# Kernel optimization log

Measured on AMD Instinct MI355X. Metric: run time of the kernel, lower is better.

The kernel has to match this reference:

```python
import jax, jax.numpy as jnp
import numpy as np

N_NODES = 100000
N_EDGES = 1600000
IN_CH = 128
HID = 32
N_GRAPHS = 64


def _gcn_conv(x, src, dst, W, b, n_nodes):
    # PyG GCNConv defaults: x' = D^{-1/2} (A + I) D^{-1/2} (x W) + b
    h = x @ W                                   # [N, out]
    loop = jnp.arange(n_nodes, dtype=src.dtype)
    s = jnp.concatenate([src, loop])            # add self-loops
    d = jnp.concatenate([dst, loop])
    deg = jax.ops.segment_sum(jnp.ones_like(d, dtype=h.dtype), d, num_segments=n_nodes)
    dinv = jnp.where(deg > 0, jax.lax.rsqrt(deg), 0.0)
    norm = dinv[s] * dinv[d]                    # [E+N]
    msg = h[s] * norm[:, None]                  # gather + scale
    out = jax.ops.segment_sum(msg, d, num_segments=n_nodes)  # scatter-add
    return out + b


def setup_inputs() -> dict:
    key = jax.random.key(0)
    ks = jax.random.split(key, 8)
    x = jax.random.normal(ks[0], (N_NODES, IN_CH), dtype=jnp.float32)
    edge_index = jax.random.randint(ks[1], (2, N_EDGES), 0, N_NODES, dtype=jnp.int32)
    batch = jnp.sort(jax.random.randint(ks[2], (N_NODES,), 0, N_GRAPHS, dtype=jnp.int32))
    W1 = jax.random.normal(ks[3], (IN_CH, HID), dtype=jnp.float32) * (1.0 / np.sqrt(IN_CH))
    b1 = jnp.zeros((HID,), dtype=jnp.float32)
    W2 = jax.random.normal(ks[4], (HID, HID), dtype=jnp.float32) * (1.0 / np.sqrt(HID))
    b2 = jnp.zeros((HID,), dtype=jnp.float32)
    Ws = jax.random.normal(ks[5], (HID, HID), dtype=jnp.float32) * (1.0 / np.sqrt(HID))
    bs = jnp.zeros((HID,), dtype=jnp.float32)
    return {"x": x, "edge_index": edge_index, "batch": batch,
            "W1": W1, "b1": b1, "W2": W2, "b2": b2, "Ws": Ws, "bs": bs}


def reference(x, edge_index, batch, W1, b1, W2, b2, Ws, bs):
    src, dst = edge_index[0], edge_index[1]
    n = x.shape[0]
    h = _gcn_conv(x, src, dst, W1, b1, n)
    h = jax.nn.relu(h)
    h = _gcn_conv(h, src, dst, W2, b2, n)       # [N, HID] node embeddings
    # global_mean_pool over graph ids
    ones = jnp.ones((n,), dtype=h.dtype)
    cnt = jax.ops.segment_sum(ones, batch, num_segments=N_GRAPHS)
    gsum = jax.ops.segment_sum(h, batch, num_segments=N_GRAPHS)
    g = gsum / jnp.maximum(cnt, 1.0)[:, None]   # [G, HID]
    summary = g @ Ws + bs
    return summary, h
```

## Files before the change

### kernel.cpp

```cpp
#include <hip/hip_runtime.h>

#define N_NODES  100000
#define N_EDGES  1600000
#define IN_CH    128
#define HID      32
#define N_GRAPHS 64

#define NBIN   391
#define CHUNK  4096
#define MGRID  391
#define STG    5120
#define LCAP   2048

#define OFF_B      0
#define OFF_EDGEPK 3200000
#define OFF_CSR    4800000
#define OFF_COLT   6400000
#define OFF_BINB   6400391
#define OFF_ROWPTR 6400784
#define OFF_DINV   6500785

__device__ __forceinline__ unsigned bfr(float f) {
    unsigned u = __float_as_uint(f);
    u += 0x7fffu + ((u >> 16) & 1u);
    return u >> 16;
}
__device__ __forceinline__ float bflo(unsigned w) { return __uint_as_float(w << 16); }
__device__ __forceinline__ float bfhi(unsigned w) { return __uint_as_float(w & 0xffff0000u); }

__global__ __launch_bounds__(512) void hist_kernel(const int* __restrict__ dst,
                                                   int* __restrict__ H) {
    __shared__ int s[512];
    int t = threadIdx.x, wg = blockIdx.x;
    s[t] = 0;
    __syncthreads();
    int e0 = wg * CHUNK, e1 = min(e0 + CHUNK, N_EDGES);
    for (int e = e0 + t; e < e1; e += 512) {
        int d = dst[e];
        if ((unsigned)d < N_NODES) atomicAdd(&s[d >> 8], 1);
    }
    __syncthreads();
    if (t < NBIN) H[t * MGRID + wg] = s[t];
}

__global__ __launch_bounds__(512) void scanrow_kernel(int* __restrict__ H,
                                                      int* __restrict__ colT) {
    __shared__ int s[512];
    int t = threadIdx.x, bin = blockIdx.x;
    s[t] = (t < MGRID) ? H[bin * MGRID + t] : 0;
    __syncthreads();
    for (int off = 1; off < 512; off <<= 1) {
        int v = (t >= off) ? s[t - off] : 0;
        __syncthreads();
        if (t >= off) s[t] += v;
        __syncthreads();
    }
    if (t < MGRID) H[bin * MGRID + t] = t ? s[t - 1] : 0;
    if (t == 0) colT[bin] = s[MGRID - 1];
}

__global__ __launch_bounds__(512) void scanbase_kernel(const int* __restrict__ colT,
                                                       int* __restrict__ binB,
                                                       int* __restrict__ row_ptr) {
    __shared__ int s[512];
    int t = threadIdx.x;
    s[t] = (t < NBIN) ? colT[t] : 0;
    __syncthreads();
    for (int off = 1; off < 512; off <<= 1) {
        int v = (t >= off) ? s[t - off] : 0;
        __syncthreads();
        if (t >= off) s[t] += v;
        __syncthreads();
    }
    if (t < NBIN) binB[t] = t ? s[t - 1] : 0;
    if (t == 0) { binB[NBIN] = s[NBIN - 1]; row_ptr[N_NODES] = s[NBIN - 1]; }
}

__global__ __launch_bounds__(512) void msplit_kernel(const int* __restrict__ src,
                                                     const int* __restrict__ dst,
                                                     const int* __restrict__ H,
                                                     const int* __restrict__ binB,
                                                     int* __restrict__ edgepk) {
    __shared__ int s[512];
    __shared__ int cur[NBIN];
    __shared__ int gb[NBIN];
    __shared__ int stage[CHUNK];
    __shared__ int gof[CHUNK];
    int t = threadIdx.x, wg = blockIdx.x;
    s[t] = 0;
    __syncthreads();
    int e0 = wg * CHUNK, e1 = min(e0 + CHUNK, N_EDGES);
    for (int e = e0 + t; e < e1; e += 512) {
        int d = dst[e];
        if ((unsigned)d < N_NODES) atomicAdd(&s[d >> 8], 1);
    }
    __syncthreads();
    for (int off = 1; off < 512; off <<= 1) {
        int v = (t >= off) ? s[t - off] : 0;
        __syncthreads();
        if (t >= off) s[t] += v;
        __syncthreads();
    }
    if (t < NBIN) {
        int lo = t ? s[t - 1] : 0;
        cur[t] = lo;
        gb[t] = binB[t] + H[t * MGRID + wg] - lo;
    }
    __syncthreads();
    for (int e = e0 + t; e < e1; e += 512) {
        int d = dst[e];
        if ((unsigned)d < N_NODES) {
            int b = d >> 8;
            int p = atomicAdd(&cur[b], 1);
            stage[p] = (src[e] << 8) | (d & 255);
            gof[p] = gb[b];
        }
    }
    __syncthreads();
    int total = s[511];
    for (int p = t; p < total; p += 512)
        edgepk[gof[p] + p] = stage[p];
}

__global__ __launch_bounds__(512) void csr2_kernel(const int* __restrict__ edgepk,
                                                   const int* __restrict__ binB,
                                                   int* __restrict__ row_ptr,
                                                   float* __restrict__ dinv,
                                                   int* __restrict__ csr) {
    __shared__ int cnt[256], s[256], cur[256];
    __shared__ int stage[STG];
    int t = threadIdx.x, bin = blockIdx.x;
    int ebase = binB[bin], eend = binB[bin + 1];
    int n = eend - ebase;
    if (t < 256) cnt[t] = 0;
    __syncthreads();
    for (int p = ebase + t; p < eend; p += 512)
        atomicAdd(&cnt[edgepk[p] & 255], 1);
    __syncthreads();
    if (t < 256) s[t] = cnt[t];
    __syncthreads();
    for (int off = 1; off < 256; off <<= 1) {
        int v = (t >= off && t < 256) ? s[t - off] : 0;
        __syncthreads();
        if (t >= off && t < 256) s[t] += v;
        __syncthreads();
    }
    if (t < 256) {
        int excl = t ? s[t - 1] : 0;
        int node = (bin << 8) + t;
        if (node < N_NODES) {
            dinv[node] = rsqrtf((float)(cnt[t] + 1));
            row_ptr[node] = ebase + excl;
        }
        cur[t] = excl;
    }
    __syncthreads();
    for (int p = ebase + t; p < eend; p += 512) {
        int w = edgepk[p];
        int l = atomicAdd(&cur[w & 255], 1);
        int sv = w >> 8;
        if (l < STG) stage[l] = sv;
        else csr[ebase + l] = sv;
    }
    __syncthreads();
    int lim = min(n, STG);
    for (int l = t; l < lim; l += 512)
        csr[ebase + l] = stage[l];
}

#define XS1 132
__global__ __launch_bounds__(256) void gemm1_kernel(const float* __restrict__ x,
                                                    const float* __restrict__ W1,
                                                    const float* __restrict__ dinv,
                                                    unsigned* __restrict__ Bu,
                                                    float* __restrict__ gz) {
    __shared__ float Wl[IN_CH * HID];
    __shared__ float xs[32 * XS1];
    int tid = threadIdx.x;
    if (blockIdx.x == 0)
        for (int q = tid; q < N_GRAPHS * HID + N_GRAPHS; q += 256) gz[q] = 0.f;
    for (int j = tid; j < IN_CH * HID / 4; j += 256)
        ((float4*)Wl)[j] = ((const float4*)W1)[j];
    int row0 = blockIdx.x * 32;
    const float4* x4 = (const float4*)(x + (size_t)row0 * IN_CH);
    for (int j = tid; j < 32 * IN_CH / 4; j += 256) {
        int r = j >> 5, k4 = j & 31;
        ((float4*)&xs[r * XS1])[k4] = x4[j];
    }
    __syncthreads();
    int r = tid >> 3, cg = (tid & 7) * 4;
    const float* xr = &xs[r * XS1];
    float4 acc = {0.f, 0.f, 0.f, 0.f};
    #pragma unroll 8
    for (int k = 0; k < IN_CH; ++k) {
        float xv = xr[k];
        float4 w = *(const float4*)&Wl[k * HID + cg];
        acc.x += xv * w.x; acc.y += xv * w.y; acc.z += xv * w.z; acc.w += xv * w.w;
    }
    int row = row0 + r;
    float dv = dinv[row];
    uint2 p;
    p.x = bfr(acc.x * dv) | (bfr(acc.y * dv) << 16);
    p.y = bfr(acc.z * dv) | (bfr(acc.w * dv) << 16);
    *(uint2*)&Bu[(size_t)row * 16 + (tid & 7) * 2] = p;
}

#define XS2 36
__global__ __launch_bounds__(256) void gemm2_kernel(const float* __restrict__ in,
                                                    const float* __restrict__ W2,
                                                    const float* __restrict__ dinv,
                                                    unsigned* __restrict__ Bu) {
    __shared__ float Wl[HID * HID];
    __shared__ float xs[32 * XS2];
    int tid = threadIdx.x;
    ((float4*)Wl)[tid] = ((const float4*)W2)[tid];
    int row0 = blockIdx.x * 32;
    const float4* in4 = (const float4*)(in + (size_t)row0 * HID);
    {
        int r = tid >> 3, k4 = tid & 7;
        ((float4*)&xs[r * XS2])[k4] = in4[tid];
    }
    __syncthreads();
    int r = tid >> 3, cg = (tid & 7) * 4;
    const float* xr = &xs[r * XS2];
    float4 acc = {0.f, 0.f, 0.f, 0.f};
    #pragma unroll
    for (int k = 0; k < HID; ++k) {
        float xv = xr[k];
        float4 w = *(const float4*)&Wl[k * HID + cg];
        acc.x += xv * w.x; acc.y += xv * w.y; acc.z += xv * w.z; acc.w += xv * w.w;
    }
    int row = row0 + r;
    float dv = dinv[row];
    uint2 p;
    p.x = bfr(acc.x * dv) | (bfr(acc.y * dv) << 16);
    p.y = bfr(acc.z * dv) | (bfr(acc.w * dv) << 16);
    *(uint2*)&Bu[(size_t)row * 16 + (tid & 7) * 2] = p;
}

__global__ __launch_bounds__(256) void layer_kernel(const unsigned* __restrict__ Bu,
                                                    const int* __restrict__ csr,
                                                    const int* __restrict__ row_ptr,
                                                    const float* __restrict__ dinv,
                                                    const float* __restrict__ bias,
                                                    float* __restrict__ out,
                                                    int relu) {
    __shared__ int sidx[LCAP];
    int tid = threadIdx.x;
    int n0 = blockIdx.x * 64;
    int nend = min(n0 + 64, N_NODES);
    int j0 = row_ptr[n0], j1 = row_ptr[nend];
    int nblk = j1 - j0;
    int staged = (nblk <= LCAP);
    if (staged)
        for (int p = tid; p < nblk; p += 256) sidx[p] = csr[j0 + p];
    __syncthreads();
    int node = n0 + (tid >> 2);
    if (node >= N_NODES) return;
    int c4 = tid & 3;
    const uint4* Br = (const uint4*)Bu;
    uint4 sw = Br[(size_t)node * 4 + c4];
    float a0 = bflo(sw.x), a1 = bfhi(sw.x);
    float a2 = bflo(sw.y), a3 = bfhi(sw.y);
    float a4 = bflo(sw.z), a5 = bfhi(sw.z);
    float a6 = bflo(sw.w), a7 = bfhi(sw.w);
    if (staged) {
        int j = row_ptr[node] - j0, re = row_ptr[node + 1] - j0;
        for (; j + 8 <= re; j += 8) {
            int s0 = sidx[j + 0], s1 = sidx[j + 1], s2 = sidx[j + 2], s3 = sidx[j + 3];
            int s4 = sidx[j + 4], s5 = sidx[j + 5], s6 = sidx[j + 6], s7 = sidx[j + 7];
            uint4 w0 = Br[(size_t)s0 * 4 + c4], w1 = Br[(size_t)s1 * 4 + c4];
            uint4 w2 = Br[(size_t)s2 * 4 + c4], w3 = Br[(size_t)s3 * 4 + c4];
            uint4 w4 = Br[(size_t)s4 * 4 + c4], w5 = Br[(size_t)s5 * 4 + c4];
            uint4 w6 = Br[(size_t)s6 * 4 + c4], w7 = Br[(size_t)s7 * 4 + c4];
            a0 += ((bflo(w0.x) + bflo(w1.x)) + (bflo(w2.x) + bflo(w3.x)))
                + ((bflo(w4.x) + bflo(w5.x)) + (bflo(w6.x) + bflo(w7.x)));
            a1 += ((bfhi(w0.x) + bfhi(w1.x)) + (bfhi(w2.x) + bfhi(w3.x)))
                + ((bfhi(w4.x) + bfhi(w5.x)) + (bfhi(w6.x) + bfhi(w7.x)));
            a2 += ((bflo(w0.y) + bflo(w1.y)) + (bflo(w2.y) + bflo(w3.y)))
                + ((bflo(w4.y) + bflo(w5.y)) + (bflo(w6.y) + bflo(w7.y)));
            a3 += ((bfhi(w0.y) + bfhi(w1.y)) + (bfhi(w2.y) + bfhi(w3.y)))
                + ((bfhi(w4.y) + bfhi(w5.y)) + (bfhi(w6.y) + bfhi(w7.y)));
            a4 += ((bflo(w0.z) + bflo(w1.z)) + (bflo(w2.z) + bflo(w3.z)))
                + ((bflo(w4.z) + bflo(w5.z)) + (bflo(w6.z) + bflo(w7.z)));
            a5 += ((bfhi(w0.z) + bfhi(w1.z)) + (bfhi(w2.z) + bfhi(w3.z)))
                + ((bfhi(w4.z) + bfhi(w5.z)) + (bfhi(w6.z) + bfhi(w7.z)));
            a6 += ((bflo(w0.w) + bflo(w1.w)) + (bflo(w2.w) + bflo(w3.w)))
                + ((bflo(w4.w) + bflo(w5.w)) + (bflo(w6.w) + bflo(w7.w)));
            a7 += ((bfhi(w0.w) + bfhi(w1.w)) + (bfhi(w2.w) + bfhi(w3.w)))
                + ((bfhi(w4.w) + bfhi(w5.w)) + (bfhi(w6.w) + bfhi(w7.w)));
        }
        if (j + 4 <= re) {
            int s0 = sidx[j], s1 = sidx[j + 1], s2 = sidx[j + 2], s3 = sidx[j + 3];
            uint4 w0 = Br[(size_t)s0 * 4 + c4], w1 = Br[(size_t)s1 * 4 + c4];
            uint4 w2 = Br[(size_t)s2 * 4 + c4], w3 = Br[(size_t)s3 * 4 + c4];
            a0 += (bflo(w0.x) + bflo(w1.x)) + (bflo(w2.x) + bflo(w3.x));
            a1 += (bfhi(w0.x) + bfhi(w1.x)) + (bfhi(w2.x) + bfhi(w3.x));
            a2 += (bflo(w0.y) + bflo(w1.y)) + (bflo(w2.y) + bflo(w3.y));
            a3 += (bfhi(w0.y) + bfhi(w1.y)) + (bfhi(w2.y) + bfhi(w3.y));
            a4 += (bflo(w0.z) + bflo(w1.z)) + (bflo(w2.z) + bflo(w3.z));
            a5 += (bfhi(w0.z) + bfhi(w1.z)) + (bfhi(w2.z) + bfhi(w3.z));
            a6 += (bflo(w0.w) + bflo(w1.w)) + (bflo(w2.w) + bflo(w3.w));
            a7 += (bfhi(w0.w) + bfhi(w1.w)) + (bfhi(w2.w) + bfhi(w3.w));
            j += 4;
        }
        for (; j < re; ++j) {
            uint4 w = Br[(size_t)sidx[j] * 4 + c4];
            a0 += bflo(w.x); a1 += bfhi(w.x);
            a2 += bflo(w.y); a3 += bfhi(w.y);
            a4 += bflo(w.z); a5 += bfhi(w.z);
            a6 += bflo(w.w); a7 += bfhi(w.w);
        }
    } else {
        int j = row_ptr[node], re = row_ptr[node + 1];
        for (; j < re; ++j) {
            uint4 w = Br[(size_t)csr[j] * 4 + c4];
            a0 += bflo(w.x); a1 += bfhi(w.x);
            a2 += bflo(w.y); a3 += bfhi(w.y);
            a4 += bflo(w.z); a5 += bfhi(w.z);
            a6 += bflo(w.w); a7 += bfhi(w.w);
        }
    }
    float dv = dinv[node];
    float4 bA = *(const float4*)&bias[8 * c4];
    float4 bB = *(const float4*)&bias[8 * c4 + 4];
    float4 o1, o2;
    o1.x = a0 * dv + bA.x; o1.y = a1 * dv + bA.y;
    o1.z = a2 * dv + bA.z; o1.w = a3 * dv + bA.w;
    o2.x = a4 * dv + bB.x; o2.y = a5 * dv + bB.y;
    o2.z = a6 * dv + bB.z; o2.w = a7 * dv + bB.w;
    if (relu) {
        o1.x = fmaxf(o1.x, 0.f); o1.y = fmaxf(o1.y, 0.f);
        o1.z = fmaxf(o1.z, 0.f); o1.w = fmaxf(o1.w, 0.f);
        o2.x = fmaxf(o2.x, 0.f); o2.y = fmaxf(o2.y, 0.f);
        o2.z = fmaxf(o2.z, 0.f); o2.w = fmaxf(o2.w, 0.f);
    }
    float* orow = out + (size_t)node * HID + 8 * c4;
    *(float4*)orow = o1;
    *(float4*)(orow + 4) = o2;
}

__global__ __launch_bounds__(256) void pool_kernel(const float* __restrict__ h,
                                                   const int* __restrict__ batch,
                                                   float* __restrict__ gsum,
                                                   float* __restrict__ cnt) {
    __shared__ float pool[N_GRAPHS * HID];
    __shared__ float cntl[N_GRAPHS];
    __shared__ int gmin, gmax;
    int t = threadIdx.x;
    for (int j = t; j < N_GRAPHS * HID; j += 256) pool[j] = 0.f;
    if (t < N_GRAPHS) cntl[t] = 0.f;
    if (t == 0) { gmin = N_GRAPHS; gmax = -1; }
    __syncthreads();
    int start = blockIdx.x * 256;
    int end = min(start + 256, N_NODES);
    int c = t & 31;
    float racc = 0.f;
    int rg = -1, rcnt = 0;
    for (int nb = start + (t >> 5); nb < end; nb += 8) {
        float v = h[(size_t)nb * HID + c];
        int g = batch[nb];
        if (g != rg) {
            if ((unsigned)rg < N_GRAPHS) {
                atomicAdd(&pool[rg * HID + c], racc);
                if (c == 0) {
                    atomicAdd(&cntl[rg], (float)rcnt);
                    atomicMin(&gmin, rg); atomicMax(&gmax, rg);
                }
            }
            rg = g; racc = v; rcnt = 1;
        } else { racc += v; ++rcnt; }
    }
    if ((unsigned)rg < N_GRAPHS) {
        atomicAdd(&pool[rg * HID + c], racc);
        if (c == 0) {
            atomicAdd(&cntl[rg], (float)rcnt);
            atomicMin(&gmin, rg); atomicMax(&gmax, rg);
        }
    }
    __syncthreads();
    int lo = gmin, hi = gmax;
    if (hi >= lo) {
        int span = (hi - lo + 1) * HID;
        for (int j = t; j < span; j += 256)
            atomicAdd(&gsum[lo * HID + j], pool[lo * HID + j]);
        for (int j = t; j <= hi - lo; j += 256)
            atomicAdd(&cnt[lo + j], cntl[lo + j]);
    }
}

__global__ void summary_kernel(const float* __restrict__ gsum, const float* __restrict__ cnt,
                               const float* __restrict__ Ws, const float* __restrict__ bs,
                               float* __restrict__ out) {
    int g = blockIdx.x, c = threadIdx.x;
    float inv = 1.f / fmaxf(cnt[g], 1.f);
    float acc = bs[c];
    #pragma unroll
    for (int k = 0; k < HID; ++k)
        acc += gsum[g * HID + k] * inv * Ws[k * HID + c];
    out[g * HID + c] = acc;
}

extern "C" void kernel_launch(void* const* d_in, const int* in_sizes, int n_in,
                              void* d_out, int out_size, void* d_ws, size_t ws_size,
                              hipStream_t stream) {
    const float* x    = (const float*)d_in[0];
    const int* edge   = (const int*)d_in[1];
    const int* src    = edge;
    const int* dst    = edge + N_EDGES;
    const int* batch  = (const int*)d_in[2];
    const float* W1   = (const float*)d_in[3];
    const float* b1   = (const float*)d_in[4];
    const float* W2   = (const float*)d_in[5];
    const float* b2   = (const float*)d_in[6];
    const float* Ws   = (const float*)d_in[7];
    const float* bs   = (const float*)d_in[8];

    float* ws      = (float*)d_ws;
    unsigned* Bu   = (unsigned*)(ws + OFF_B);
    int*   H       = (int*)(ws + OFF_B);
    int*   edgepk  = (int*)(ws + OFF_EDGEPK);
    int*   csr     = (int*)(ws + OFF_CSR);
    int*   colT    = (int*)(ws + OFF_COLT);
    int*   binB    = (int*)(ws + OFF_BINB);
    int*   row_ptr = (int*)(ws + OFF_ROWPTR);
    float* dinv    = ws + OFF_DINV;
    float* gsum    = ws + OFF_EDGEPK;
    float* cnt     = gsum + N_GRAPHS * HID;

    float* out     = (float*)d_out;
    float* out_sum = out;
    float* out_h   = out + N_GRAPHS * HID;

    hist_kernel    <<<MGRID, 512, 0, stream>>>(dst, H);
    scanrow_kernel <<<NBIN,  512, 0, stream>>>(H, colT);
    scanbase_kernel<<<1,     512, 0, stream>>>(colT, binB, row_ptr);
    msplit_kernel  <<<MGRID, 512, 0, stream>>>(src, dst, H, binB, edgepk);
    csr2_kernel    <<<NBIN,  512, 0, stream>>>(edgepk, binB, row_ptr, dinv, csr);

    int lgrid = (N_NODES + 63) / 64;

    gemm1_kernel<<<N_NODES / 32, 256, 0, stream>>>(x, W1, dinv, Bu, gsum);
    layer_kernel<<<lgrid, 256, 0, stream>>>(Bu, csr, row_ptr, dinv, b1, out_h, 1);

    gemm2_kernel<<<N_NODES / 32, 256, 0, stream>>>(out_h, W2, dinv, Bu);
    layer_kernel<<<lgrid, 256, 0, stream>>>(Bu, csr, row_ptr, dinv, b2, out_h, 0);

    pool_kernel<<<NBIN, 256, 0, stream>>>(out_h, batch, gsum, cnt);
    summary_kernel<<<N_GRAPHS, HID, 0, stream>>>(gsum, cnt, Ws, bs, out_sum);
}
```

Before: 223.7 us.

## Replace histogram+scan binning with atomic per-bin slot allocation into fixed-capacity bins

Drops the separate histogram and two-level scan kernels. Each chunk block now reserves space in a fixed-capacity per-bin region (BINC slots) with a global atomicAdd on a per-bin cursor, and a single small scan over the bin totals then produces the CSR offsets. This removes one full pass over dst and two launches, at the cost of global atomics, a memset, and a fixed bin capacity that could overflow if any 256-node bin gets more than 5120 edges. Edge order within a bin becomes nondeterministic, so the floating-point summation order can vary between runs.

Measured after the change: 226.2 us. About the same (+1.1%).

```diff
diff --git a/kernel.cpp b/kernel.cpp
--- a/kernel.cpp
+++ b/kernel.cpp
@@ -9,16 +9,17 @@
 #define NBIN   391
 #define CHUNK  4096
 #define MGRID  391
+#define BINC   5120
 #define STG    5120
 #define LCAP   2048
 
 #define OFF_B      0
-#define OFF_EDGEPK 3200000
-#define OFF_CSR    4800000
-#define OFF_COLT   6400000
-#define OFF_BINB   6400391
-#define OFF_ROWPTR 6400784
-#define OFF_DINV   6500785
+#define OFF_EDGEPK 1600000
+#define OFF_CSR    3700000
+#define OFF_BINCUR 5300000
+#define OFF_BINB   5300391
+#define OFF_ROWPTR 5300784
+#define OFF_DINV   5400785
 
 __device__ __forceinline__ unsigned bfr(float f) {
     unsigned u = __float_as_uint(f);
@@ -28,59 +29,10 @@
 __device__ __forceinline__ float bflo(unsigned w) { return __uint_as_float(w << 16); }
 __device__ __forceinline__ float bfhi(unsigned w) { return __uint_as_float(w & 0xffff0000u); }
 
-__global__ __launch_bounds__(512) void hist_kernel(const int* __restrict__ dst,
-                                                   int* __restrict__ H) {
-    __shared__ int s[512];
-    int t = threadIdx.x, wg = blockIdx.x;
-    s[t] = 0;
-    __syncthreads();
-    int e0 = wg * CHUNK, e1 = min(e0 + CHUNK, N_EDGES);
-    for (int e = e0 + t; e < e1; e += 512) {
-        int d = dst[e];
-        if ((unsigned)d < N_NODES) atomicAdd(&s[d >> 8], 1);
-    }
-    __syncthreads();
-    if (t < NBIN) H[t * MGRID + wg] = s[t];
-}
-
-__global__ __launch_bounds__(512) void scanrow_kernel(int* __restrict__ H,
-                                                      int* __restrict__ colT) {
-    __shared__ int s[512];
-    int t = threadIdx.x, bin = blockIdx.x;
-    s[t] = (t < MGRID) ? H[bin * MGRID + t] : 0;
-    __syncthreads();
-    for (int off = 1; off < 512; off <<= 1) {
-        int v = (t >= off) ? s[t - off] : 0;
-        __syncthreads();
-        if (t >= off) s[t] += v;
-        __syncthreads();
-    }
-    if (t < MGRID) H[bin * MGRID + t] = t ? s[t - 1] : 0;
-    if (t == 0) colT[bin] = s[MGRID - 1];
-}
-
-__global__ __launch_bounds__(512) void scanbase_kernel(const int* __restrict__ colT,
-                                                       int* __restrict__ binB,
-                                                       int* __restrict__ row_ptr) {
-    __shared__ int s[512];
-    int t = threadIdx.x;
-    s[t] = (t < NBIN) ? colT[t] : 0;
-    __syncthreads();
-    for (int off = 1; off < 512; off <<= 1) {
-        int v = (t >= off) ? s[t - off] : 0;
-        __syncthreads();
-        if (t >= off) s[t] += v;
-        __syncthreads();
-    }
-    if (t < NBIN) binB[t] = t ? s[t - 1] : 0;
-    if (t == 0) { binB[NBIN] = s[NBIN - 1]; row_ptr[N_NODES] = s[NBIN - 1]; }
-}
-
-__global__ __launch_bounds__(512) void msplit_kernel(const int* __restrict__ src,
-                                                     const int* __restrict__ dst,
-                                                     const int* __restrict__ H,
-                                                     const int* __restrict__ binB,
-                                                     int* __restrict__ edgepk) {
+__global__ __launch_bounds__(512) void msplit2_kernel(const int* __restrict__ src,
+                                                      const int* __restrict__ dst,
+                                                      int* __restrict__ bincur,
+                                                      int* __restrict__ edgepk) {
     __shared__ int s[512];
     __shared__ int cur[NBIN];
     __shared__ int gb[NBIN];
@@ -103,8 +55,10 @@
     }
     if (t < NBIN) {
         int lo = t ? s[t - 1] : 0;
+        int cnt = s[t] - lo;
         cur[t] = lo;
-        gb[t] = binB[t] + H[t * MGRID + wg] - lo;
+        int base = cnt ? atomicAdd(&bincur[t], cnt) : 0;
+        gb[t] = t * BINC + base - lo;
     }
     __syncthreads();
     for (int e = e0 + t; e < e1; e += 512) {
@@ -120,6 +74,23 @@
     int total = s[511];
     for (int p = t; p < total; p += 512)
         edgepk[gof[p] + p] = stage[p];
+}
+
+__global__ __launch_bounds__(512) void scanb_kernel(const int* __restrict__ bincur,
+                                                    int* __restrict__ binB,
+                                                    int* __restrict__ row_ptr) {
+    __shared__ int s[512];
+    int t = threadIdx.x;
+    s[t] = (t < NBIN) ? bincur[t] : 0;
+    __syncthreads();
+    for (int off = 1; off < 512; off <<= 1) {
+        int v = (t >= off) ? s[t - off] : 0;
+        __syncthreads();
+        if (t >= off) s[t] += v;
+        __syncthreads();
+    }
+    if (t < NBIN) binB[t] = t ? s[t - 1] : 0;
+    if (t == 0) { binB[NBIN] = s[NBIN - 1]; row_ptr[N_NODES] = s[NBIN - 1]; }
 }
 
 __global__ __launch_bounds__(512) void csr2_kernel(const int* __restrict__ edgepk,
@@ -130,12 +101,13 @@
     __shared__ int cnt[256], s[256], cur[256];
     __shared__ int stage[STG];
     int t = threadIdx.x, bin = blockIdx.x;
-    int ebase = binB[bin], eend = binB[bin + 1];
-    int n = eend - ebase;
+    int obase = binB[bin];
+    int n = binB[bin + 1] - obase;
+    int pb = bin * BINC;
     if (t < 256) cnt[t] = 0;
     __syncthreads();
-    for (int p = ebase + t; p < eend; p += 512)
-        atomicAdd(&cnt[edgepk[p] & 255], 1);
+    for (int p = t; p < n; p += 512)
+        atomicAdd(&cnt[edgepk[pb + p] & 255], 1);
     __syncthreads();
     if (t < 256) s[t] = cnt[t];
     __syncthreads();
@@ -150,22 +122,22 @@
         int node = (bin << 8) + t;
         if (node < N_NODES) {
             dinv[node] = rsqrtf((float)(cnt[t] + 1));
-            row_ptr[node] = ebase + excl;
+            row_ptr[node] = obase + excl;
         }
         cur[t] = excl;
     }
     __syncthreads();
-    for (int p = ebase + t; p < eend; p += 512) {
-        int w = edgepk[p];
+    for (int p = t; p < n; p += 512) {
+        int w = edgepk[pb + p];
         int l = atomicAdd(&cur[w & 255], 1);
         int sv = w >> 8;
         if (l < STG) stage[l] = sv;
-        else csr[ebase + l] = sv;
+        else csr[obase + l] = sv;
     }
     __syncthreads();
     int lim = min(n, STG);
     for (int l = t; l < lim; l += 512)
-        csr[ebase + l] = stage[l];
+        csr[obase + l] = stage[l];
 }
 
 #define XS1 132
@@ -418,10 +390,9 @@
 
     float* ws      = (float*)d_ws;
     unsigned* Bu   = (unsigned*)(ws + OFF_B);
-    int*   H       = (int*)(ws + OFF_B);
     int*   edgepk  = (int*)(ws + OFF_EDGEPK);
     int*   csr     = (int*)(ws + OFF_CSR);
-    int*   colT    = (int*)(ws + OFF_COLT);
+    int*   bincur  = (int*)(ws + OFF_BINCUR);
     int*   binB    = (int*)(ws + OFF_BINB);
     int*   row_ptr = (int*)(ws + OFF_ROWPTR);
     float* dinv    = ws + OFF_DINV;
@@ -432,11 +403,10 @@
     float* out_sum = out;
     float* out_h   = out + N_GRAPHS * HID;
 
-    hist_kernel    <<<MGRID, 512, 0, stream>>>(dst, H);
-    scanrow_kernel <<<NBIN,  512, 0, stream>>>(H, colT);
-    scanbase_kernel<<<1,     512, 0, stream>>>(colT, binB, row_ptr);
-    msplit_kernel  <<<MGRID, 512, 0, stream>>>(src, dst, H, binB, edgepk);
-    csr2_kernel    <<<NBIN,  512, 0, stream>>>(edgepk, binB, row_ptr, dinv, csr);
+    hipMemsetAsync(bincur, 0, NBIN * sizeof(int), stream);
+    msplit2_kernel<<<MGRID, 512, 0, stream>>>(src, dst, bincur, edgepk);
+    scanb_kernel  <<<1,     512, 0, stream>>>(bincur, binB, row_ptr);
+    csr2_kernel   <<<NBIN,  512, 0, stream>>>(edgepk, binB, row_ptr, dinv, csr);
 
     int lgrid = (N_NODES + 63) / 64;
 
```
